# Kernel optimization log

Measured on AMD Instinct MI355X. Metric: run time of the kernel, lower is better.

The kernel has to match this reference:

```python
import jax, jax.numpy as jnp
import numpy as np
import math

B, S, D, H, L, V, EXP = 2, 2048, 1024, 16, 6, 32000, 4
HD = D // H
LN_EPS = 1e-5


def _positional_encoding(seq_len, d):
    # Faithful to the (nonstandard) source: pe[p, 2i] = sin(p / 10000**(2*(2i)/d)),
    # pe[p, 2i+1] = cos(p / 10000**(2*(2i+1)/d))  (note: exponent uses the raw column index i, doubled)
    pos = jnp.arange(seq_len, dtype=jnp.float32)[:, None]            # [S,1]
    i_even = jnp.arange(0, d, 2, dtype=jnp.float32)                  # even column indices
    i_odd = i_even + 1.0
    inv_even = jnp.power(10000.0, -2.0 * i_even / d)
    inv_odd = jnp.power(10000.0, -2.0 * i_odd / d)
    pe = jnp.zeros((seq_len, d), dtype=jnp.float32)
    pe = pe.at[:, 0::2].set(jnp.sin(pos * inv_even))
    pe = pe.at[:, 1::2].set(jnp.cos(pos * inv_odd))
    return pe  # [S, D]


def _layernorm(x, g, b):
    mu = jnp.mean(x, axis=-1, keepdims=True)
    var = jnp.mean((x - mu) ** 2, axis=-1, keepdims=True)
    return (x - mu) * jax.lax.rsqrt(var + LN_EPS) * g + b


def _mha(h, Wq, Wk, Wv, Wo, bo):
    # h: [B,S,D]; no mask (mask is None in the source's encoder path)
    q = (h @ Wq).reshape(B, S, H, HD)
    k = (h @ Wk).reshape(B, S, H, HD)
    v = (h @ Wv).reshape(B, S, H, HD)
    scores = jnp.einsum('bqhd,bkhd->bhqk', q, k) / math.sqrt(HD)
    attn = jax.nn.softmax(scores, axis=-1)
    out = jnp.einsum('bhqk,bkhd->bqhd', attn, v).reshape(B, S, D)
    return out @ Wo + bo


def setup_inputs() -> dict:
    key = jax.random.key(0)
    ks = jax.random.split(key, 12)
    sd = 0.02
    inp = {
        'x': jax.random.randint(ks[0], (B, S), 0, V),
        'embed': jax.random.normal(ks[1], (V, D), jnp.float32) * sd,
        'Wq': jax.random.normal(ks[2], (L, D, D), jnp.float32) * sd,
        'Wk': jax.random.normal(ks[3], (L, D, D), jnp.float32) * sd,
        'Wv': jax.random.normal(ks[4], (L, D, D), jnp.float32) * sd,
        'Wo': jax.random.normal(ks[5], (L, D, D), jnp.float32) * sd,
        'bo': jnp.zeros((L, D), jnp.float32),
        'ln1_g': jnp.ones((L, D), jnp.float32),
        'ln1_b': jnp.zeros((L, D), jnp.float32),
        'W1': jax.random.normal(ks[6], (L, D, EXP * D), jnp.float32) * sd,
        'b1': jnp.zeros((L, EXP * D), jnp.float32),
        'W2': jax.random.normal(ks[7], (L, EXP * D, D), jnp.float32) * sd,
        'b2': jnp.zeros((L, D), jnp.float32),
        'ln2_g': jnp.ones((L, D), jnp.float32),
        'ln2_b': jnp.zeros((L, D), jnp.float32),
    }
    return inp


def reference(x, embed, Wq, Wk, Wv, Wo, bo, ln1_g, ln1_b, W1, b1, W2, b2, ln2_g, ln2_b):
    h = embed[x]                                   # [B,S,D] token embedding
    h = h * math.sqrt(D) + _positional_encoding(S, D)[None]
    for l in range(L):
        attn = _mha(h, Wq[l], Wk[l], Wv[l], Wo[l], bo[l])
        n1 = _layernorm(attn + h, ln1_g[l], ln1_b[l])          # dropout is identity at eval
        ff = jax.nn.relu(n1 @ W1[l] + b1[l]) @ W2[l] + b2[l]
        h = _layernorm(ff + n1, ln2_g[l], ln2_b[l])
    return h
```

## Files before the change

### kernel.cpp

```cpp
#include <hip/hip_runtime.h>
#include <hip/hip_bf16.h>
#include <math.h>

#define B_ 2
#define S_ 2048
#define D_ 1024
#define H_ 16
#define HD_ 64
#define L_ 6
#define NTOK (B_*S_)

typedef unsigned short ushort_t;
typedef unsigned int uint_t;

typedef __attribute__((ext_vector_type(8))) short bf16x8;
typedef __attribute__((ext_vector_type(4))) float f32x4;

__device__ __forceinline__ float bf2f(ushort_t u) {
    return __uint_as_float(((uint_t)u) << 16);
}
__device__ __forceinline__ ushort_t f2bf(float f) {
    uint_t x = __float_as_uint(f);
    uint_t r = (x + 0x7FFFu + ((x >> 16) & 1u)) >> 16;
    return (ushort_t)r;
}

__device__ __forceinline__ void gld_lds16(const ushort_t* g, ushort_t* l) {
    __builtin_amdgcn_global_load_lds(
        (const __attribute__((address_space(1))) unsigned int*)g,
        (__attribute__((address_space(3))) unsigned int*)l,
        16, 0, 0);
}

__global__ __launch_bounds__(256) void cvtT_kernel(const float* __restrict__ in,
                                                   ushort_t* __restrict__ out,
                                                   int K, int N) {
    __shared__ float tile[32][33];
    int n0 = blockIdx.x * 32;
    int k0 = blockIdx.y * 32;
    int t = threadIdx.x;
    int tc = t & 31, tr = t >> 5;
#pragma unroll
    for (int i = 0; i < 4; i++) {
        int k = k0 + tr + i * 8;
        tile[tr + i * 8][tc] = in[(size_t)k * N + n0 + tc];
    }
    __syncthreads();
#pragma unroll
    for (int i = 0; i < 4; i++) {
        int n = n0 + tr + i * 8;
        out[(size_t)n * K + k0 + tc] = f2bf(tile[tc][tr + i * 8]);
    }
}

__global__ void embed_kernel(const int* __restrict__ x, const float* __restrict__ emb,
                             float* __restrict__ h, ushort_t* __restrict__ hb) {
    int row = blockIdx.x;
    int s = row % S_;
    int tok = x[row];
    const float* erow = emb + (size_t)tok * D_;
    float* hrow = h + (size_t)row * D_;
    ushort_t* hbrow = hb + (size_t)row * D_;
    const float kExp = -2.0f * 13.287712379549449f / (float)D_;
    for (int c = threadIdx.x; c < D_; c += blockDim.x) {
        float factor = exp2f(kExp * (float)c);
        float ang = (float)s * factor;
        float pe = (c & 1) ? cosf(ang) : sinf(ang);
        float v = erow[c] * 32.0f + pe;
        hrow[c] = v;
        hbrow[c] = f2bf(v);
    }
}

#define GEMM_OUT_BF16 1
#define GEMM_RELU 2

template<int BM>
__global__ __launch_bounds__(256) void gemm_kernel(
    const ushort_t* __restrict__ A, const ushort_t* __restrict__ Bt,
    const float* __restrict__ bias, void* __restrict__ out,
    int M, int N, int K, int flags)
{
    constexpr int MI = BM / 32;
    __shared__ __align__(16) ushort_t sA[BM * 32];
    __shared__ __align__(16) ushort_t sB[128 * 32];

    int t = threadIdx.x;
    int lane = t & 63, w = t >> 6;
    int ln15 = lane & 15, q = lane >> 4;
    int n0 = blockIdx.x * 128, m0 = blockIdx.y * BM;
    int wr = w >> 1, wc = w & 1;

    f32x4 acc[MI][4];
#pragma unroll
    for (int i = 0; i < MI; i++)
#pragma unroll
        for (int j = 0; j < 4; j++) acc[i][j] = (f32x4){0.f, 0.f, 0.f, 0.f};

    const ushort_t* aPtr = A + (size_t)(m0 + w * (BM / 4) + (lane >> 2)) * K + (lane & 3) * 8;
    const ushort_t* bPtr = Bt + (size_t)(n0 + w * 32 + (lane >> 2)) * K + (lane & 3) * 8;
    ushort_t* sAw = sA + w * (BM / 4) * 32;
    ushort_t* sBw = sB + w * 1024;

    for (int k0 = 0; k0 < K; k0 += 32) {
        __syncthreads();
        gld_lds16(aPtr, sAw);
        if constexpr (BM == 128) gld_lds16(aPtr + 16 * K, sAw + 512);
        gld_lds16(bPtr, sBw);
        gld_lds16(bPtr + 16 * K, sBw + 512);
        aPtr += 32; bPtr += 32;
        __syncthreads();

        bf16x8 af[MI], bfr[4];
#pragma unroll
        for (int i = 0; i < MI; i++)
            af[i] = *(const bf16x8*)(sA + (wr * (BM / 2) + i * 16 + ln15) * 32 + q * 8);
#pragma unroll
        for (int i = 0; i < 4; i++)
            bfr[i] = *(const bf16x8*)(sB + (wc * 64 + i * 16 + ln15) * 32 + q * 8);
#pragma unroll
        for (int mi = 0; mi < MI; mi++)
#pragma unroll
            for (int ni = 0; ni < 4; ni++)
                acc[mi][ni] = __builtin_amdgcn_mfma_f32_16x16x32_bf16(
                    af[mi], bfr[ni], acc[mi][ni], 0, 0, 0);
    }

#pragma unroll
    for (int mi = 0; mi < MI; mi++) {
#pragma unroll
        for (int ni = 0; ni < 4; ni++) {
            int row = m0 + wr * (BM / 2) + mi * 16 + q * 4;
            int col = n0 + wc * 64 + ni * 16 + ln15;
            float bv = bias ? bias[col] : 0.f;
#pragma unroll
            for (int r = 0; r < 4; r++) {
                float v = acc[mi][ni][r] + bv;
                if (flags & GEMM_RELU) v = fmaxf(v, 0.f);
                if (flags & GEMM_OUT_BF16)
                    ((ushort_t*)out)[(size_t)(row + r) * N + col] = f2bf(v);
                else
                    ((float*)out)[(size_t)(row + r) * N + col] = v;
            }
        }
    }
}

#define SKP 72

__global__ __launch_bounds__(256) void attn_kernel(
    const ushort_t* __restrict__ Q, const ushort_t* __restrict__ Km,
    const ushort_t* __restrict__ Vm, int ld, ushort_t* __restrict__ O)
{
    __shared__ __align__(16) ushort_t sK[64 * SKP];
    __shared__ __align__(16) ushort_t sVt[64 * SKP];
    __shared__ __align__(16) ushort_t sP[4][16 * SKP];

    int t = threadIdx.x;
    int w = t >> 6, lane = t & 63;
    int ln15 = lane & 15, q = lane >> 4;
    int b = blockIdx.z, hh = blockIdx.y;
    int q0 = blockIdx.x * 64;

    const size_t base = (size_t)b * S_ * ld + hh * HD_;
    const size_t obase = (size_t)b * S_ * D_ + hh * HD_;

    bf16x8 aq[2];
    {
        const ushort_t* qrow = Q + base + (size_t)(q0 + w * 16 + ln15) * ld;
        aq[0] = *(const bf16x8*)(qrow + q * 8);
        aq[1] = *(const bf16x8*)(qrow + 32 + q * 8);
    }

    f32x4 accO[4];
#pragma unroll
    for (int i = 0; i < 4; i++) accO[i] = (f32x4){0.f, 0.f, 0.f, 0.f};
    float mrow[4] = {-1e30f, -1e30f, -1e30f, -1e30f};
    float lrow[4] = {0.f, 0.f, 0.f, 0.f};

    int kkey = t >> 3, khd = (t & 7) * 8;
    int vkey = t & 63, vhd = (t >> 6) * 8;

    for (int k0 = 0; k0 < S_; k0 += 64) {
        uint4 kv0 = *(const uint4*)(Km + base + (size_t)(k0 + kkey) * ld + khd);
        uint4 kv1 = *(const uint4*)(Km + base + (size_t)(k0 + 32 + kkey) * ld + khd);
        uint4 vv0 = *(const uint4*)(Vm + base + (size_t)(k0 + vkey) * ld + vhd);
        uint4 vv1 = *(const uint4*)(Vm + base + (size_t)(k0 + vkey) * ld + 32 + vhd);
        __syncthreads();
        *(uint4*)(&sK[kkey * SKP + khd]) = kv0;
        *(uint4*)(&sK[(kkey + 32) * SKP + khd]) = kv1;
        const ushort_t* vp0 = (const ushort_t*)&vv0;
        const ushort_t* vp1 = (const ushort_t*)&vv1;
#pragma unroll
        for (int j = 0; j < 8; j++) {
            sVt[(vhd + j) * SKP + vkey] = vp0[j];
            sVt[(vhd + 32 + j) * SKP + vkey] = vp1[j];
        }
        __syncthreads();

        f32x4 sc[4];
#pragma unroll
        for (int nb = 0; nb < 4; nb++) {
            bf16x8 bk0 = *(const bf16x8*)(&sK[(nb * 16 + ln15) * SKP + q * 8]);
            bf16x8 bk1 = *(const bf16x8*)(&sK[(nb * 16 + ln15) * SKP + 32 + q * 8]);
            f32x4 z = (f32x4){0.f, 0.f, 0.f, 0.f};
            z = __builtin_amdgcn_mfma_f32_16x16x32_bf16(aq[0], bk0, z, 0, 0, 0);
            z = __builtin_amdgcn_mfma_f32_16x16x32_bf16(aq[1], bk1, z, 0, 0, 0);
            sc[nb] = z;
        }

        float p[4][4];
#pragma unroll
        for (int r = 0; r < 4; r++) {
            float s0 = sc[0][r] * 0.125f, s1 = sc[1][r] * 0.125f;
            float s2 = sc[2][r] * 0.125f, s3 = sc[3][r] * 0.125f;
            float pm = fmaxf(fmaxf(s0, s1), fmaxf(s2, s3));
#pragma unroll
            for (int off = 1; off < 16; off <<= 1)
                pm = fmaxf(pm, __shfl_xor(pm, off));
            float mnew = fmaxf(mrow[r], pm);
            float alpha = __expf(mrow[r] - mnew);
            mrow[r] = mnew;
            float p0 = __expf(s0 - mnew), p1 = __expf(s1 - mnew);
            float p2 = __expf(s2 - mnew), p3 = __expf(s3 - mnew);
            p[0][r] = p0; p[1][r] = p1; p[2][r] = p2; p[3][r] = p3;
            lrow[r] = lrow[r] * alpha + (p0 + p1 + p2 + p3);
            accO[0][r] *= alpha; accO[1][r] *= alpha;
            accO[2][r] *= alpha; accO[3][r] *= alpha;
        }

#pragma unroll
        for (int nb = 0; nb < 4; nb++)
#pragma unroll
            for (int r = 0; r < 4; r++)
                sP[w][(q * 4 + r) * SKP + nb * 16 + ln15] = f2bf(p[nb][r]);

#pragma unroll
        for (int c = 0; c < 2; c++) {
            bf16x8 ap = *(const bf16x8*)(&sP[w][ln15 * SKP + c * 32 + q * 8]);
#pragma unroll
            for (int nhd = 0; nhd < 4; nhd++) {
                bf16x8 bv = *(const bf16x8*)(&sVt[(nhd * 16 + ln15) * SKP + c * 32 + q * 8]);
                accO[nhd] = __builtin_amdgcn_mfma_f32_16x16x32_bf16(ap, bv, accO[nhd], 0, 0, 0);
            }
        }
    }

    float inv[4];
#pragma unroll
    for (int r = 0; r < 4; r++) {
        float l = lrow[r];
#pragma unroll
        for (int off = 1; off < 16; off <<= 1)
            l += __shfl_xor(l, off);
        inv[r] = 1.0f / l;
    }
    ushort_t* ob = O + obase;
#pragma unroll
    for (int nhd = 0; nhd < 4; nhd++)
#pragma unroll
        for (int r = 0; r < 4; r++)
            ob[(size_t)(q0 + w * 16 + q * 4 + r) * D_ + nhd * 16 + ln15] =
                f2bf(accO[nhd][r] * inv[r]);
}

__global__ __launch_bounds__(256) void ln_add_kernel(
    const float* __restrict__ a, const float* __restrict__ bres,
    const float* __restrict__ g, const float* __restrict__ be,
    float* __restrict__ of, ushort_t* __restrict__ ob)
{
    int row = blockIdx.x;
    int t = threadIdx.x;
    const float* ar = a + (size_t)row * D_;
    const float* br = bres + (size_t)row * D_;
    float x[4];
    float s = 0.f, sq = 0.f;
#pragma unroll
    for (int i = 0; i < 4; i++) {
        int c = t + i * 256;
        float v = ar[c] + br[c];
        x[i] = v; s += v; sq += v * v;
    }
#pragma unroll
    for (int off = 32; off; off >>= 1) {
        s += __shfl_xor(s, off);
        sq += __shfl_xor(sq, off);
    }
    __shared__ float rs[4], rq[4];
    int w = t >> 6;
    if ((t & 63) == 0) { rs[w] = s; rq[w] = sq; }
    __syncthreads();
    s = rs[0] + rs[1] + rs[2] + rs[3];
    sq = rq[0] + rq[1] + rq[2] + rq[3];
    float mu = s * (1.0f / D_);
    float var = sq * (1.0f / D_) - mu * mu;
    float rstd = rsqrtf(var + 1e-5f);
#pragma unroll
    for (int i = 0; i < 4; i++) {
        int c = t + i * 256;
        float y = (x[i] - mu) * rstd * g[c] + be[c];
        of[(size_t)row * D_ + c] = y;
        ob[(size_t)row * D_ + c] = f2bf(y);
    }
}

extern "C" void kernel_launch(void* const* d_in, const int* in_sizes, int n_in,
                              void* d_out, int out_size, void* d_ws, size_t ws_size,
                              hipStream_t stream) {
    const int*   x    = (const int*)d_in[0];
    const float* emb  = (const float*)d_in[1];
    const float* Wq   = (const float*)d_in[2];
    const float* Wk   = (const float*)d_in[3];
    const float* Wv   = (const float*)d_in[4];
    const float* Wo   = (const float*)d_in[5];
    const float* bo   = (const float*)d_in[6];
    const float* ln1g = (const float*)d_in[7];
    const float* ln1b = (const float*)d_in[8];
    const float* W1   = (const float*)d_in[9];
    const float* b1   = (const float*)d_in[10];
    const float* W2   = (const float*)d_in[11];
    const float* b2   = (const float*)d_in[12];
    const float* ln2g = (const float*)d_in[13];
    const float* ln2b = (const float*)d_in[14];

    char* ws = (char*)d_ws;
    float*    h    = (float*)(ws + 0);
    ushort_t* hb   = (ushort_t*)(ws + 16777216);
    float*    t0   = (float*)(ws + 25165824);
    float*    n1   = (float*)(ws + 41943040);
    ushort_t* n1b  = (ushort_t*)(ws + 58720256);
    ushort_t* qkvb = (ushort_t*)(ws + 67108864);
    ushort_t* ab   = (ushort_t*)(ws + 92274688);
    ushort_t* ff1  = (ushort_t*)(ws + 67108864);
    ushort_t* wqkvT= (ushort_t*)(ws + 100663296);
    ushort_t* woT  = (ushort_t*)(ws + 106954752);
    ushort_t* w1T  = (ushort_t*)(ws + 109051904);
    ushort_t* w2T  = (ushort_t*)(ws + 117440512);

    embed_kernel<<<NTOK, 256, 0, stream>>>(x, emb, h, hb);

    for (int l = 0; l < L_; l++) {
        const float* Wq_l = Wq + (size_t)l * D_ * D_;
        const float* Wk_l = Wk + (size_t)l * D_ * D_;
        const float* Wv_l = Wv + (size_t)l * D_ * D_;
        const float* Wo_l = Wo + (size_t)l * D_ * D_;
        const float* bo_l = bo + (size_t)l * D_;
        const float* W1_l = W1 + (size_t)l * D_ * 4 * D_;
        const float* b1_l = b1 + (size_t)l * 4 * D_;
        const float* W2_l = W2 + (size_t)l * 4 * D_ * D_;
        const float* b2_l = b2 + (size_t)l * D_;

        cvtT_kernel<<<dim3(32, 32), 256, 0, stream>>>(Wq_l, wqkvT,                 1024, 1024);
        cvtT_kernel<<<dim3(32, 32), 256, 0, stream>>>(Wk_l, wqkvT + 1024 * 1024,   1024, 1024);
        cvtT_kernel<<<dim3(32, 32), 256, 0, stream>>>(Wv_l, wqkvT + 2048 * 1024,   1024, 1024);
        cvtT_kernel<<<dim3(32, 32), 256, 0, stream>>>(Wo_l, woT,                   1024, 1024);
        cvtT_kernel<<<dim3(128, 32), 256, 0, stream>>>(W1_l, w1T,                  1024, 4096);
        cvtT_kernel<<<dim3(32, 128), 256, 0, stream>>>(W2_l, w2T,                  4096, 1024);

        gemm_kernel<128><<<dim3(3072 / 128, NTOK / 128), 256, 0, stream>>>(
            hb, wqkvT, nullptr, qkvb, NTOK, 3072, 1024, GEMM_OUT_BF16);

        attn_kernel<<<dim3(S_ / 64, H_, B_), 256, 0, stream>>>(
            qkvb, qkvb + 1024, qkvb + 2048, 3072, ab);

        gemm_kernel<64><<<dim3(1024 / 128, NTOK / 64), 256, 0, stream>>>(
            ab, woT, bo_l, t0, NTOK, 1024, 1024, 0);
        ln_add_kernel<<<NTOK, 256, 0, stream>>>(t0, h, ln1g + l * D_, ln1b + l * D_, n1, n1b);

        gemm_kernel<128><<<dim3(4096 / 128, NTOK / 128), 256, 0, stream>>>(
            n1b, w1T, b1_l, ff1, NTOK, 4096, 1024, GEMM_OUT_BF16 | GEMM_RELU);
        gemm_kernel<64><<<dim3(1024 / 128, NTOK / 64), 256, 0, stream>>>(
            ff1, w2T, b2_l, t0, NTOK, 1024, 4096, 0);

        float* of = (l == L_ - 1) ? (float*)d_out : h;
        ln_add_kernel<<<NTOK, 256, 0, stream>>>(t0, n1, ln2g + l * D_, ln2b + l * D_, of, hb);
    }
}
```

Before: 2.416 ms.

## Load attention K/V fragments directly from global with pre-transposed V

Adds a kernel that transposes V per (batch, head) into a head-dim-major buffer. The attention kernel then drops its shared-memory K/V staging and both barriers, reading MFMA operand fragments straight from global memory (K rows, transposed V rows). A swizzled 1-D grid maps the 8 blocks likely sharing an XCD to the same (batch, head), so K/V stay hot in L2. This removes the LDS transpose stores and syncs, but adds a separate transpose pass, relies on cache hits for repeated K/V reads across waves, and reuses the t0 workspace region for the transposed V.

```diff
diff --git a/kernel.cpp b/kernel.cpp
--- a/kernel.cpp
+++ b/kernel.cpp
@@ -51,6 +51,26 @@
         int n = n0 + tr + i * 8;
         out[(size_t)n * K + k0 + tc] = f2bf(tile[tc][tr + i * 8]);
     }
+}
+
+__global__ __launch_bounds__(256) void vt_kernel(const ushort_t* __restrict__ v,
+                                                 ushort_t* __restrict__ vt) {
+    __shared__ ushort_t tile[32][34];
+    int s0 = blockIdx.x * 32;
+    int hd0 = (blockIdx.y & 1) * 32;
+    int bh = blockIdx.y >> 1;
+    int b = bh >> 4, h = bh & 15;
+    int t = threadIdx.x;
+    int tc = t & 31, tr = t >> 5;
+    const ushort_t* src = v + (size_t)(b * S_ + s0) * 3072 + 2048 + h * 64 + hd0;
+#pragma unroll
+    for (int i = 0; i < 4; i++)
+        tile[tr + i * 8][tc] = src[(size_t)(tr + i * 8) * 3072 + tc];
+    __syncthreads();
+    ushort_t* dst = vt + ((size_t)bh * 64 + hd0) * S_ + s0;
+#pragma unroll
+    for (int i = 0; i < 4; i++)
+        dst[(size_t)(tr + i * 8) * S_ + tc] = tile[tc][tr + i * 8];
 }
 
 __global__ void embed_kernel(const int* __restrict__ x, const float* __restrict__ emb,
@@ -149,25 +169,29 @@
 #define SKP 72
 
 __global__ __launch_bounds__(256) void attn_kernel(
-    const ushort_t* __restrict__ Q, const ushort_t* __restrict__ Km,
-    const ushort_t* __restrict__ Vm, int ld, ushort_t* __restrict__ O)
+    const ushort_t* __restrict__ Qm, const ushort_t* __restrict__ Km,
+    const ushort_t* __restrict__ Vt, ushort_t* __restrict__ O)
 {
-    __shared__ __align__(16) ushort_t sK[64 * SKP];
-    __shared__ __align__(16) ushort_t sVt[64 * SKP];
     __shared__ __align__(16) ushort_t sP[4][16 * SKP];
 
     int t = threadIdx.x;
     int w = t >> 6, lane = t & 63;
     int ln15 = lane & 15, q = lane >> 4;
-    int b = blockIdx.z, hh = blockIdx.y;
-    int q0 = blockIdx.x * 64;
-
-    const size_t base = (size_t)b * S_ * ld + hh * HD_;
+
+    int wg = blockIdx.x;
+    int lin = (wg & 7) * 128 + (wg >> 3);
+    int bh = lin >> 5;
+    int qblk = lin & 31;
+    int b = bh >> 4, hh = bh & 15;
+    int q0 = qblk * 64;
+
+    const size_t base  = (size_t)b * S_ * 3072 + hh * HD_;
+    const size_t vbase = (size_t)bh * HD_ * S_;
     const size_t obase = (size_t)b * S_ * D_ + hh * HD_;
 
     bf16x8 aq[2];
     {
-        const ushort_t* qrow = Q + base + (size_t)(q0 + w * 16 + ln15) * ld;
+        const ushort_t* qrow = Qm + base + (size_t)(q0 + w * 16 + ln15) * 3072;
         aq[0] = *(const bf16x8*)(qrow + q * 8);
         aq[1] = *(const bf16x8*)(qrow + 32 + q * 8);
     }
@@ -178,31 +202,13 @@
     float mrow[4] = {-1e30f, -1e30f, -1e30f, -1e30f};
     float lrow[4] = {0.f, 0.f, 0.f, 0.f};
 
-    int kkey = t >> 3, khd = (t & 7) * 8;
-    int vkey = t & 63, vhd = (t >> 6) * 8;
-
     for (int k0 = 0; k0 < S_; k0 += 64) {
-        uint4 kv0 = *(const uint4*)(Km + base + (size_t)(k0 + kkey) * ld + khd);
-        uint4 kv1 = *(const uint4*)(Km + base + (size_t)(k0 + 32 + kkey) * ld + khd);
-        uint4 vv0 = *(const uint4*)(Vm + base + (size_t)(k0 + vkey) * ld + vhd);
-        uint4 vv1 = *(const uint4*)(Vm + base + (size_t)(k0 + vkey) * ld + 32 + vhd);
-        __syncthreads();
-        *(uint4*)(&sK[kkey * SKP + khd]) = kv0;
-        *(uint4*)(&sK[(kkey + 32) * SKP + khd]) = kv1;
-        const ushort_t* vp0 = (const ushort_t*)&vv0;
-        const ushort_t* vp1 = (const ushort_t*)&vv1;
-#pragma unroll
-        for (int j = 0; j < 8; j++) {
-            sVt[(vhd + j) * SKP + vkey] = vp0[j];
-            sVt[(vhd + 32 + j) * SKP + vkey] = vp1[j];
-        }
-        __syncthreads();
-
         f32x4 sc[4];
 #pragma unroll
         for (int nb = 0; nb < 4; nb++) {
-            bf16x8 bk0 = *(const bf16x8*)(&sK[(nb * 16 + ln15) * SKP + q * 8]);
-            bf16x8 bk1 = *(const bf16x8*)(&sK[(nb * 16 + ln15) * SKP + 32 + q * 8]);
+            const ushort_t* krow = Km + base + (size_t)(k0 + nb * 16 + ln15) * 3072;
+            bf16x8 bk0 = *(const bf16x8*)(krow + q * 8);
+            bf16x8 bk1 = *(const bf16x8*)(krow + 32 + q * 8);
             f32x4 z = (f32x4){0.f, 0.f, 0.f, 0.f};
             z = __builtin_amdgcn_mfma_f32_16x16x32_bf16(aq[0], bk0, z, 0, 0, 0);
             z = __builtin_amdgcn_mfma_f32_16x16x32_bf16(aq[1], bk1, z, 0, 0, 0);
@@ -240,7 +246,9 @@
             bf16x8 ap = *(const bf16x8*)(&sP[w][ln15 * SKP + c * 32 + q * 8]);
 #pragma unroll
             for (int nhd = 0; nhd < 4; nhd++) {
-                bf16x8 bv = *(const bf16x8*)(&sVt[(nhd * 16 + ln15) * SKP + c * 32 + q * 8]);
+                const ushort_t* vrow = Vt + vbase + (size_t)(nhd * 16 + ln15) * S_
+                                       + k0 + c * 32 + q * 8;
+                bf16x8 bv = *(const bf16x8*)vrow;
                 accO[nhd] = __builtin_amdgcn_mfma_f32_16x16x32_bf16(ap, bv, accO[nhd], 0, 0, 0);
             }
         }
@@ -327,6 +335,7 @@
     float*    h    = (float*)(ws + 0);
     ushort_t* hb   = (ushort_t*)(ws + 16777216);
     float*    t0   = (float*)(ws + 25165824);
+    ushort_t* vtb  = (ushort_t*)(ws + 25165824);
     float*    n1   = (float*)(ws + 41943040);
     ushort_t* n1b  = (ushort_t*)(ws + 58720256);
     ushort_t* qkvb = (ushort_t*)(ws + 67108864);
@@ -360,8 +369,9 @@
         gemm_kernel<128><<<dim3(3072 / 128, NTOK / 128), 256, 0, stream>>>(
             hb, wqkvT, nullptr, qkvb, NTOK, 3072, 1024, GEMM_OUT_BF16);
 
-        attn_kernel<<<dim3(S_ / 64, H_, B_), 256, 0, stream>>>(
-            qkvb, qkvb + 1024, qkvb + 2048, 3072, ab);
+        vt_kernel<<<dim3(S_ / 32, 64), 256, 0, stream>>>(qkvb, vtb);
+
+        attn_kernel<<<1024, 256, 0, stream>>>(qkvb, qkvb + 1024, vtb, ab);
 
         gemm_kernel<64><<<dim3(1024 / 128, NTOK / 64), 256, 0, stream>>>(
             ab, woT, bo_l, t0, NTOK, 1024, 1024, 0);
```

Measured after the change: 3.131 ms. +29.6%, slower.
